# Optimization experiments

Measured on AMD Instinct MI355X. Metric: run time of the kernel, lower is better.

## Reference

```python
import jax, jax.numpy as jnp
import numpy as np

B, N, HID, H = 16, 256, 512, 8
DK = HID // H          # att_size = 64
FEAT = 8               # storage/operator feature dim
MLP_H = 64             # interaction MLP hidden dim
LAM = 0.1              # htap_lambda
SCALE = DK ** -0.5


def _pair_bias(feat, W1, b1, W2, b2):
    """MLP([v_i || v_j || |v_i - v_j|]) for all pairs -> [B,N,N,H].
    Split W1 over the three concat blocks so the per-node parts are O(N)."""
    F = feat.shape[-1]
    Wa, Wb, Wc = W1[:F], W1[F:2 * F], W1[2 * F:]
    hi = feat @ Wa                                    # [B,N,MLP_H]
    hj = feat @ Wb                                    # [B,N,MLP_H]
    diff = jnp.abs(feat[:, :, None, :] - feat[:, None, :, :])  # [B,N,N,F]
    h = jax.nn.relu(hi[:, :, None, :] + hj[:, None, :, :] + diff @ Wc + b1)
    return h @ W2 + b2                                # [B,N,N,H]


def setup_inputs() -> dict:
    key = jax.random.key(0)
    ks = jax.random.split(key, 24)
    g = lambda i, shape, s=0.05: jax.random.normal(ks[i], shape, jnp.float32) * (1.0 if s is None else 1.0) * (s / 0.05 * 0.05 if False else 1.0)
    def w(i, shape, scale):
        return jax.random.normal(ks[i], shape, jnp.float32) * scale
    inp = {
        "q": w(0, (B, N, HID), 1.0),
        "k": w(1, (B, N, HID), 1.0),
        "v": w(2, (B, N, HID), 1.0),
        "tree_attn_bias": w(3, (B, H, N, N), 1.0),
        "storage_features": w(4, (B, N, FEAT), 1.0),
        "operator_features": w(5, (B, N, FEAT), 1.0),
        # attention projections (stored as [in,out])
        "Wq": w(6, (HID, HID), HID ** -0.5), "bq": jnp.zeros((HID,), jnp.float32),
        "Wk": w(7, (HID, HID), HID ** -0.5), "bk": jnp.zeros((HID,), jnp.float32),
        "Wv": w(8, (HID, HID), HID ** -0.5), "bv": jnp.zeros((HID,), jnp.float32),
        "Wo": w(9, (HID, HID), HID ** -0.5), "bo": jnp.zeros((HID,), jnp.float32),
        # f_s interaction MLP: Linear(3*FEAT,64) -> ReLU -> Linear(64,H)
        "fs_W1": w(10, (3 * FEAT, MLP_H), (3 * FEAT) ** -0.5), "fs_b1": jnp.zeros((MLP_H,), jnp.float32),
        "fs_W2": w(11, (MLP_H, H), MLP_H ** -0.5), "fs_b2": jnp.zeros((H,), jnp.float32),
        # f_o interaction MLP
        "fo_W1": w(12, (3 * FEAT, MLP_H), (3 * FEAT) ** -0.5), "fo_b1": jnp.zeros((MLP_H,), jnp.float32),
        "fo_W2": w(13, (MLP_H, H), MLP_H ** -0.5), "fo_b2": jnp.zeros((H,), jnp.float32),
    }
    return inp


def reference(q, k, v, tree_attn_bias, storage_features, operator_features,
              Wq, bq, Wk, bk, Wv, bv, Wo, bo,
              fs_W1, fs_b1, fs_W2, fs_b2, fo_W1, fo_b1, fo_W2, fo_b2):
    # projections -> [B,H,N,DK]
    qh = (q @ Wq + bq).reshape(B, N, H, DK).transpose(0, 2, 1, 3) * SCALE
    kh = (k @ Wk + bk).reshape(B, N, H, DK).transpose(0, 2, 1, 3)
    vh = (v @ Wv + bv).reshape(B, N, H, DK).transpose(0, 2, 1, 3)

    scores = jnp.einsum("bhnd,bhmd->bhnm", qh, kh) + tree_attn_bias

    htap = (_pair_bias(storage_features, fs_W1, fs_b1, fs_W2, fs_b2)
            + _pair_bias(operator_features, fo_W1, fo_b1, fo_W2, fo_b2))  # [B,N,N,H]
    scores = scores + LAM * htap.transpose(0, 3, 1, 2)

    attn = jax.nn.softmax(scores, axis=-1)            # dropout rate 0 (eval)
    x = jnp.einsum("bhnm,bhmd->bhnd", attn, vh)
    x = x.transpose(0, 2, 1, 3).reshape(B, N, HID)
    return x @ Wo + bo
```

## Files before the change

kernel.cpp:

```cpp
#include <hip/hip_runtime.h>
#include <hip/hip_bf16.h>
#include <stdint.h>

#define B_    16
#define N_    256
#define HID_  512
#define H_    8
#define DK_   64
#define FEAT_ 8
#define MLPH_ 64
#define LAM_  0.1f
#define SCALE_ 0.125f

typedef short bf16x8 __attribute__((ext_vector_type(8)));
typedef float f32x4  __attribute__((ext_vector_type(4)));

union U8 { uint4 u; bf16x8 h; ushort s[8]; };

__device__ __forceinline__ uint16_t f32_to_bf16(float x) {
    uint32_t u = __float_as_uint(x);
    u += 0x7fffu + ((u >> 16) & 1u);
    return (uint16_t)(u >> 16);
}
__device__ __forceinline__ float bf16_to_f32(uint16_t v) {
    return __uint_as_float(((uint32_t)v) << 16);
}
__device__ __forceinline__ uint32_t pk_bf16(float lo, float hi) {
    float2 xy; xy.x = lo; xy.y = hi;
    __hip_bfloat162 b2 = __float22bfloat162_rn(xy);
    return *(uint32_t*)&b2;
}
#define LDS_FENCE() asm volatile("s_waitcnt lgkmcnt(0)" ::: "memory")

__global__ __launch_bounds__(256, 4) void proj_kernel(
    const float* __restrict__ q, const float* __restrict__ k, const float* __restrict__ v,
    const float* __restrict__ Wq, const float* __restrict__ bq,
    const float* __restrict__ Wk, const float* __restrict__ bk,
    const float* __restrict__ Wv, const float* __restrict__ bv,
    ushort* __restrict__ qh, ushort* __restrict__ kh, ushort* __restrict__ vh)
{
    int z = blockIdx.z;
    const float* X    = (z == 0) ? q  : (z == 1) ? k  : v;
    const float* W    = (z == 0) ? Wq : (z == 1) ? Wk : Wv;
    const float* bias = (z == 0) ? bq : (z == 1) ? bk : bv;
    ushort* out       = (z == 0) ? qh : (z == 1) ? kh : vh;
    float scale       = (z == 0) ? SCALE_ : 1.0f;

    int m0 = blockIdx.x * 128;
    int h  = blockIdx.y;
    int c0 = h * 64;

    __shared__ __align__(16) ushort Xs[2][128 * 40];
    __shared__ __align__(16) ushort Ws[2][64 * 40];

    int t = threadIdx.x;
    int wave = t >> 6, lane = t & 63;
    int l15 = lane & 15, qd = lane >> 4;

    int xr = t >> 1, xc = (t & 1) * 16;
    int kr = t & 15, nq = t >> 4;

    f32x4 acc0[4] = {}, acc1[4] = {};

    float4 xv[4], w0, w1;
    #pragma unroll
    for (int p = 0; p < 4; p++)
        xv[p] = *(const float4*)&X[(m0 + xr) * HID_ + xc + p * 4];
    w0 = *(const float4*)&W[(2 * kr) * HID_ + c0 + nq * 4];
    w1 = *(const float4*)&W[(2 * kr + 1) * HID_ + c0 + nq * 4];

    for (int k0 = 0; k0 < HID_; k0 += 32) {
        int buf = (k0 >> 5) & 1;
        #pragma unroll
        for (int p = 0; p < 4; p++) {
            ushort4 o;
            o.x = f32_to_bf16(xv[p].x); o.y = f32_to_bf16(xv[p].y);
            o.z = f32_to_bf16(xv[p].z); o.w = f32_to_bf16(xv[p].w);
            *(ushort4*)&Xs[buf][xr * 40 + xc + p * 4] = o;
        }
        {
            const float* a0 = &w0.x; const float* a1 = &w1.x;
            #pragma unroll
            for (int i = 0; i < 4; i++) {
                uint32_t pk = (uint32_t)f32_to_bf16(a0[i]) | ((uint32_t)f32_to_bf16(a1[i]) << 16);
                *(uint32_t*)&Ws[buf][(nq * 4 + i) * 40 + 2 * kr] = pk;
            }
        }
        __syncthreads();

        if (k0 + 32 < HID_) {
            int kn = k0 + 32;
            #pragma unroll
            for (int p = 0; p < 4; p++)
                xv[p] = *(const float4*)&X[(m0 + xr) * HID_ + kn + xc + p * 4];
            w0 = *(const float4*)&W[(kn + 2 * kr) * HID_ + c0 + nq * 4];
            w1 = *(const float4*)&W[(kn + 2 * kr + 1) * HID_ + c0 + nq * 4];
        }

        bf16x8 af0 = *(const bf16x8*)&Xs[buf][(wave * 32 + l15) * 40 + qd * 8];
        bf16x8 af1 = *(const bf16x8*)&Xs[buf][(wave * 32 + 16 + l15) * 40 + qd * 8];
        #pragma unroll
        for (int nt = 0; nt < 4; nt++) {
            bf16x8 bf = *(const bf16x8*)&Ws[buf][(nt * 16 + l15) * 40 + qd * 8];
            acc0[nt] = __builtin_amdgcn_mfma_f32_16x16x32_bf16(af0, bf, acc0[nt], 0, 0, 0);
            acc1[nt] = __builtin_amdgcn_mfma_f32_16x16x32_bf16(af1, bf, acc1[nt], 0, 0, 0);
        }
    }

    #pragma unroll
    for (int nt = 0; nt < 4; nt++) {
        float bb = bias[c0 + nt * 16 + l15];
        #pragma unroll
        for (int g = 0; g < 2; g++) {
            const f32x4& a = g ? acc1[nt] : acc0[nt];
            #pragma unroll
            for (int r = 0; r < 4; r++) {
                int m = m0 + wave * 32 + g * 16 + qd * 4 + r;
                int b_ = m >> 8, n_ = m & 255;
                float val = (a[r] + bb) * scale;
                out[(((b_ * H_ + h) * N_) + n_) * DK_ + nt * 16 + l15] = f32_to_bf16(val);
            }
        }
    }
}

__global__ void prep_frags(const float* __restrict__ fsW1, const float* __restrict__ foW1,
                           const float* __restrict__ fsW2, const float* __restrict__ foW2,
                           uint4* __restrict__ bfrag1, uint4* __restrict__ bfrag2)
{
    int t = threadIdx.x;
    #pragma unroll
    for (int e = t; e < 512; e += 256) {
        int nt = e >> 6, lane = e & 63, l15 = lane & 15, qd = lane >> 4;
        int n = nt * 16 + l15;
        ushort vals[8];
        #pragma unroll
        for (int u = 0; u < 8; u++) {
            float x = 0.f;
            if (n < 64) {
                if (qd == 0) x = fsW1[(16 + u) * 64 + n];
                else if (qd == 1) x = fsW1[(8 + u) * 64 + n];
            } else {
                int n2 = n - 64;
                if (qd == 2) x = foW1[(16 + u) * 64 + n2];
                else if (qd == 3) x = foW1[(8 + u) * 64 + n2];
            }
            vals[u] = f32_to_bf16(x);
        }
        uint4 pk;
        pk.x = (uint32_t)vals[0] | ((uint32_t)vals[1] << 16);
        pk.y = (uint32_t)vals[2] | ((uint32_t)vals[3] << 16);
        pk.z = (uint32_t)vals[4] | ((uint32_t)vals[5] << 16);
        pk.w = (uint32_t)vals[6] | ((uint32_t)vals[7] << 16);
        bfrag1[e] = pk;
    }
    {
        int e = t;
        int ks = e >> 6, lane = e & 63, l15 = lane & 15, qd = lane >> 4;
        ushort vals[8];
        #pragma unroll
        for (int u = 0; u < 8; u++) {
            float x = 0.f;
            if (l15 < 8) {
                int k2 = ks * 32 + qd * 8 + u;
                int c = ((k2 & 7) << 4) | (k2 >> 3);
                x = LAM_ * ((c < 64) ? fsW2[c * 8 + l15] : foW2[(c - 64) * 8 + l15]);
            }
            vals[u] = f32_to_bf16(x);
        }
        uint4 pk;
        pk.x = (uint32_t)vals[0] | ((uint32_t)vals[1] << 16);
        pk.y = (uint32_t)vals[2] | ((uint32_t)vals[3] << 16);
        pk.z = (uint32_t)vals[4] | ((uint32_t)vals[5] << 16);
        pk.w = (uint32_t)vals[6] | ((uint32_t)vals[7] << 16);
        bfrag2[e] = pk;
    }
}

#define HSTRIDE 136
__global__ __launch_bounds__(256, 4) void pair_bias_mfma(
    const float* __restrict__ sf, const float* __restrict__ of,
    const float* __restrict__ fsW1, const float* __restrict__ fsb1,
    const float* __restrict__ foW1, const float* __restrict__ fob1,
    const float* __restrict__ fsb2, const float* __restrict__ fob2,
    const uint4* __restrict__ bfrag1, const uint4* __restrict__ bfrag2,
    ushort* __restrict__ mlpb)
{
    __shared__ __align__(16) ushort hbuf[4][16 * HSTRIDE];
    __shared__ float hisbuf[128];
    __shared__ __align__(4) ushort tbuf[4][8 * 16];

    int i = blockIdx.x, b = blockIdx.y;
    int t = threadIdx.x;
    int wave = t >> 6, lane = t & 63;
    int l15 = lane & 15, qd = lane >> 4;

    if (t < 128) {
        int set = t >> 6, kk = t & 63;
        const float* W1 = set ? foW1 : fsW1;
        const float* fi = (set ? of : sf) + (b * N_ + i) * FEAT_;
        float a = (set ? fob1 : fsb1)[kk];
        #pragma unroll
        for (int f = 0; f < FEAT_; f++) a += fi[f] * W1[f * 64 + kk];
        hisbuf[t] = a;
    }

    bf16x8 Bf1[8], Bf2[4];
    #pragma unroll
    for (int nt = 0; nt < 8; nt++) { U8 u; u.u = bfrag1[nt * 64 + lane]; Bf1[nt] = u.h; }
    #pragma unroll
    for (int ks = 0; ks < 4; ks++) { U8 u; u.u = bfrag2[ks * 64 + lane]; Bf2[ks] = u.h; }

    const float* fsr = sf + (b * N_ + i) * FEAT_;
    const float* forr = of + (b * N_ + i) * FEAT_;
    float fsi[8], foi[8];
    #pragma unroll
    for (int u = 0; u < 8; u++) { fsi[u] = fsr[u]; foi[u] = forr[u]; }
    float b2l = LAM_ * (fsb2[l15 & 7] + fob2[l15 & 7]);

    __syncthreads();

    float hv[8];
    #pragma unroll
    for (int nt = 0; nt < 8; nt++) hv[nt] = hisbuf[nt * 16 + l15];

    ushort* hb = hbuf[wave];
    #pragma unroll
    for (int qt = 0; qt < 4; qt++) {
        int j0 = (wave * 4 + qt) * 16;
        int j = j0 + l15;

        const float* fr = ((qd < 2) ? sf : of) + (b * N_ + j) * FEAT_;
        float4 f0 = *(const float4*)&fr[0];
        float4 f1 = *(const float4*)&fr[4];
        float vals[8] = {f0.x, f0.y, f0.z, f0.w, f1.x, f1.y, f1.z, f1.w};
        if ((qd & 1) == 0) {
            const float* fi = (qd < 2) ? fsi : foi;
            #pragma unroll
            for (int u = 0; u < 8; u++) vals[u] = fabsf(vals[u] - fi[u]);
        }
        U8 au;
        #pragma unroll
        for (int p = 0; p < 4; p++)
            ((uint32_t*)&au)[p] = pk_bf16(vals[2 * p], vals[2 * p + 1]);
        bf16x8 af = au.h;

        f32x4 S1[8];
        #pragma unroll
        for (int nt = 0; nt < 8; nt++) {
            f32x4 c0 = {hv[nt], hv[nt], hv[nt], hv[nt]};
            S1[nt] = __builtin_amdgcn_mfma_f32_16x16x32_bf16(af, Bf1[nt], c0, 0, 0, 0);
        }

        #pragma unroll
        for (int r = 0; r < 4; r++) {
            uint4 w;
            w.x = pk_bf16(fmaxf(S1[0][r], 0.f), fmaxf(S1[1][r], 0.f));
            w.y = pk_bf16(fmaxf(S1[2][r], 0.f), fmaxf(S1[3][r], 0.f));
            w.z = pk_bf16(fmaxf(S1[4][r], 0.f), fmaxf(S1[5][r], 0.f));
            w.w = pk_bf16(fmaxf(S1[6][r], 0.f), fmaxf(S1[7][r], 0.f));
            *(uint4*)&hb[(qd * 4 + r) * HSTRIDE + l15 * 8] = w;
        }
        LDS_FENCE();

        f32x4 S2 = {b2l, b2l, b2l, b2l};
        #pragma unroll
        for (int ks = 0; ks < 4; ks++) {
            bf16x8 a2 = *(const bf16x8*)&hb[l15 * HSTRIDE + ks * 32 + qd * 8];
            S2 = __builtin_amdgcn_mfma_f32_16x16x32_bf16(a2, Bf2[ks], S2, 0, 0, 0);
        }

        if (l15 < 8) {
            #pragma unroll
            for (int r = 0; r < 4; r++)
                tbuf[wave][l15 * 16 + qd * 4 + r] = f32_to_bf16(S2[r]);
        }
        LDS_FENCE();

        {
            int h2 = lane >> 3, jp = lane & 7;
            uint32_t lo = tbuf[wave][h2 * 16 + jp * 2];
            uint32_t hi = tbuf[wave][h2 * 16 + jp * 2 + 1];
            uint32_t pk = lo | (hi << 16);
            *(uint32_t*)&mlpb[(((size_t)(b * H_ + h2) * N_ + i) * N_) + j0 + jp * 2] = pk;
        }
    }
}

__global__ __launch_bounds__(256, 2) void attn_kernel(
    const ushort* __restrict__ qh, const ushort* __restrict__ kh,
    const ushort* __restrict__ vh, const float* __restrict__ tree,
    const ushort* __restrict__ mlpb, ushort* __restrict__ ctxb)
{
    __shared__ __align__(16) ushort bufKP[256 * 72];
    __shared__ __align__(16) ushort bufV[64 * 264];

    int blk = blockIdx.x;
    int bh = blk >> 2;
    int quarter = blk & 3;

    int t = threadIdx.x;
    int wave = t >> 6, lane = t & 63;
    int l15 = lane & 15, qd = lane >> 4;
    int i0w = quarter * 64 + wave * 16;

    const ushort* khb = kh + (size_t)bh * N_ * DK_;
    const ushort* vhb = vh + (size_t)bh * N_ * DK_;

    #pragma unroll
    for (int u = t; u < 2048; u += 256) {
        int j = u >> 3, seg = (u & 7) * 8;
        uint4 kv = *(const uint4*)&khb[j * DK_ + seg];
        *(uint4*)&bufKP[j * 72 + seg] = kv;
    }
    #pragma unroll
    for (int u = t; u < 1024; u += 256) {
        int rp = u & 127, d0 = (u >> 7) * 8;
        U8 v0, v1;
        v0.u = *(const uint4*)&vhb[(2 * rp) * DK_ + d0];
        v1.u = *(const uint4*)&vhb[(2 * rp + 1) * DK_ + d0];
        #pragma unroll
        for (int jj = 0; jj < 8; jj++) {
            uint32_t pk = (uint32_t)v0.s[jj] | ((uint32_t)v1.s[jj] << 16);
            *(uint32_t*)&bufV[(d0 + jj) * 264 + 2 * rp] = pk;
        }
    }
    __syncthreads();

    bf16x8 a0, a1;
    {
        size_t qb = ((size_t)bh * N_ + i0w + l15) * DK_;
        U8 t0, t1;
        t0.u = *(const uint4*)&qh[qb + qd * 8];
        t1.u = *(const uint4*)&qh[qb + 32 + qd * 8];
        a0 = t0.h; a1 = t1.h;
    }
    f32x4 S[16];
    #pragma unroll
    for (int nt = 0; nt < 16; nt++) {
        f32x4 acc = {};
        bf16x8 b0 = *(const bf16x8*)&bufKP[(nt * 16 + l15) * 72 + qd * 8];
        bf16x8 b1 = *(const bf16x8*)&bufKP[(nt * 16 + l15) * 72 + 32 + qd * 8];
        acc = __builtin_amdgcn_mfma_f32_16x16x32_bf16(a0, b0, acc, 0, 0, 0);
        acc = __builtin_amdgcn_mfma_f32_16x16x32_bf16(a1, b1, acc, 0, 0, 0);
        S[nt] = acc;
    }

    {
        size_t base = ((size_t)bh * N_ + i0w + qd * 4) * N_ + l15;
        const float*  tr = tree + base;
        const ushort* mb = mlpb + base;
        #pragma unroll
        for (int nt = 0; nt < 16; nt++)
            #pragma unroll
            for (int r = 0; r < 4; r++)
                S[nt][r] += tr[(size_t)r * N_ + nt * 16] + bf16_to_f32(mb[(size_t)r * N_ + nt * 16]);
    }

    float mx[4], sm[4];
    #pragma unroll
    for (int r = 0; r < 4; r++) mx[r] = -1e30f;
    #pragma unroll
    for (int nt = 0; nt < 16; nt++)
        #pragma unroll
        for (int r = 0; r < 4; r++) mx[r] = fmaxf(mx[r], S[nt][r]);
    #pragma unroll
    for (int r = 0; r < 4; r++) {
        #pragma unroll
        for (int m = 1; m <= 8; m <<= 1) mx[r] = fmaxf(mx[r], __shfl_xor(mx[r], m));
    }
    #pragma unroll
    for (int r = 0; r < 4; r++) sm[r] = 0.f;
    #pragma unroll
    for (int nt = 0; nt < 16; nt++)
        #pragma unroll
        for (int r = 0; r < 4; r++) {
            float e = __expf(S[nt][r] - mx[r]);
            S[nt][r] = e;
            sm[r] += e;
        }
    #pragma unroll
    for (int r = 0; r < 4; r++) {
        #pragma unroll
        for (int m = 1; m <= 8; m <<= 1) sm[r] += __shfl_xor(sm[r], m);
        sm[r] = 1.0f / sm[r];
    }

    __syncthreads();

    {
        uint32_t* Pw = (uint32_t*)&bufKP[wave * 16 * 264];
        #pragma unroll
        for (int nt = 0; nt < 16; nt++)
            #pragma unroll
            for (int r = 0; r < 4; r++) {
                float p = S[nt][r] * sm[r];
                float po = __shfl_xor(p, 1);
                uint32_t pk = (uint32_t)f32_to_bf16(p) | ((uint32_t)f32_to_bf16(po) << 16);
                if ((lane & 1) == 0)
                    Pw[(qd * 4 + r) * 132 + nt * 8 + (l15 >> 1)] = pk;
            }
    }
    __syncthreads();

    const ushort* Pw = &bufKP[wave * 16 * 264];
    f32x4 O[4] = {};
    #pragma unroll
    for (int ks = 0; ks < 8; ks++) {
        int j0 = ks * 32;
        bf16x8 pa = *(const bf16x8*)&Pw[l15 * 264 + j0 + qd * 8];
        #pragma unroll
        for (int ntd = 0; ntd < 4; ntd++) {
            bf16x8 vb = *(const bf16x8*)&bufV[(ntd * 16 + l15) * 264 + j0 + qd * 8];
            O[ntd] = __builtin_amdgcn_mfma_f32_16x16x32_bf16(pa, vb, O[ntd], 0, 0, 0);
        }
    }

    #pragma unroll
    for (int ntd = 0; ntd < 4; ntd++)
        #pragma unroll
        for (int r = 0; r < 4; r++)
            ctxb[((size_t)bh * N_ + i0w + qd * 4 + r) * DK_ + ntd * 16 + l15] =
                f32_to_bf16(O[ntd][r]);
}

__global__ __launch_bounds__(256, 4) void outproj_kernel(
    const ushort* __restrict__ ctxb, const float* __restrict__ Wo,
    const float* __restrict__ bo, float* __restrict__ out)
{
    int m0 = blockIdx.x * 64;
    int c0 = blockIdx.y * 64;

    __shared__ __align__(16) ushort Xs[64 * 40];
    __shared__ __align__(16) ushort Ws[64 * 40];

    int t = threadIdx.x;
    int wave = t >> 6, lane = t & 63;
    int l15 = lane & 15, qd = lane >> 4;

    f32x4 acc[4] = {};

    for (int k0 = 0; k0 < HID_; k0 += 32) {
        __syncthreads();
        {
            int r = t >> 2, s8 = (t & 3) * 8;
            int m = m0 + r, b_ = m >> 8, n_ = m & 255;
            uint4 xv = *(const uint4*)&ctxb[(((b_ * H_ + (k0 >> 6)) * N_) + n_) * DK_ + (k0 & 63) + s8];
            *(uint4*)&Xs[r * 40 + s8] = xv;
        }
        {
            int kr = t & 15, nq = t >> 4;
            float4 w0 = *(const float4*)&Wo[(k0 + 2 * kr) * HID_ + c0 + nq * 4];
            float4 w1 = *(const float4*)&Wo[(k0 + 2 * kr + 1) * HID_ + c0 + nq * 4];
            const float* a0 = &w0.x; const float* a1 = &w1.x;
            #pragma unroll
            for (int i = 0; i < 4; i++) {
                uint32_t pk = (uint32_t)f32_to_bf16(a0[i]) | ((uint32_t)f32_to_bf16(a1[i]) << 16);
                *(uint32_t*)&Ws[(nq * 4 + i) * 40 + 2 * kr] = pk;
            }
        }
        __syncthreads();
        bf16x8 af = *(const bf16x8*)&Xs[(wave * 16 + l15) * 40 + qd * 8];
        #pragma unroll
        for (int nt = 0; nt < 4; nt++) {
            bf16x8 bf = *(const bf16x8*)&Ws[(nt * 16 + l15) * 40 + qd * 8];
            acc[nt] = __builtin_amdgcn_mfma_f32_16x16x32_bf16(af, bf, acc[nt], 0, 0, 0);
        }
    }

    #pragma unroll
    for (int nt = 0; nt < 4; nt++) {
        float bb = bo[c0 + nt * 16 + l15];
        #pragma unroll
        for (int r = 0; r < 4; r++) {
            int m = m0 + wave * 16 + qd * 4 + r;
            out[m * HID_ + c0 + nt * 16 + l15] = acc[nt][r] + bb;
        }
    }
}

extern "C" void kernel_launch(void* const* d_in, const int* in_sizes, int n_in,
                              void* d_out, int out_size, void* d_ws, size_t ws_size,
                              hipStream_t stream)
{
    const float* q    = (const float*)d_in[0];
    const float* k    = (const float*)d_in[1];
    const float* v    = (const float*)d_in[2];
    const float* tree = (const float*)d_in[3];
    const float* sf   = (const float*)d_in[4];
    const float* of   = (const float*)d_in[5];
    const float* Wq   = (const float*)d_in[6];
    const float* bq   = (const float*)d_in[7];
    const float* Wk   = (const float*)d_in[8];
    const float* bk   = (const float*)d_in[9];
    const float* Wv   = (const float*)d_in[10];
    const float* bv   = (const float*)d_in[11];
    const float* Wo   = (const float*)d_in[12];
    const float* bo   = (const float*)d_in[13];
    const float* fsW1 = (const float*)d_in[14];
    const float* fsb1 = (const float*)d_in[15];
    const float* fsW2 = (const float*)d_in[16];
    const float* fsb2 = (const float*)d_in[17];
    const float* foW1 = (const float*)d_in[18];
    const float* fob1 = (const float*)d_in[19];
    const float* foW2 = (const float*)d_in[20];
    const float* fob2 = (const float*)d_in[21];

    char* ws = (char*)d_ws;
    ushort* qh     = (ushort*)(ws + 0);
    ushort* kh     = (ushort*)(ws + 4194304);
    ushort* vh     = (ushort*)(ws + 8388608);
    ushort* ctxb   = (ushort*)(ws + 12582912);
    uint4*  bfrag1 = (uint4*)(ws + 16777216);
    uint4*  bfrag2 = (uint4*)(ws + 16785408);
    ushort* mlpb   = (ushort*)(ws + 23080960);

    proj_kernel<<<dim3(32, 8, 3), 256, 0, stream>>>(q, k, v, Wq, bq, Wk, bk, Wv, bv, qh, kh, vh);
    prep_frags<<<1, 256, 0, stream>>>(fsW1, foW1, fsW2, foW2, bfrag1, bfrag2);
    pair_bias_mfma<<<dim3(N_, B_), 256, 0, stream>>>(sf, of, fsW1, fsb1, foW1, fob1,
                                                     fsb2, fob2, bfrag1, bfrag2, mlpb);
    attn_kernel<<<512, 256, 0, stream>>>(qh, kh, vh, tree, mlpb, ctxb);
    outproj_kernel<<<dim3(64, 8), 256, 0, stream>>>(ctxb, Wo, bo, (float*)d_out);
}
```

Measured before the change: 226.4 us.

## Software-pipeline pair-bias MLP stages with double-buffered LDS per wave

Restructures the pair_bias kernel so that all four A-fragments are loaded from global before the barrier. The first-layer MFMAs for the next 16-column tile are issued while the second-layer MFMAs and the store for the current tile run, using double-buffered hidden and transpose LDS buffers. The aim is to hide MFMA and LDS latency within each wave. In exchange it uses more registers and twice the LDS, and lowers the launch_bounds occupancy hint from 4 to 3 blocks.

```diff
diff --git a/kernel.cpp b/kernel.cpp
--- a/kernel.cpp
+++ b/kernel.cpp
@@ -178,7 +178,7 @@
 }
 
 #define HSTRIDE 136
-__global__ __launch_bounds__(256, 4) void pair_bias_mfma(
+__global__ __launch_bounds__(256, 3) void pair_bias_mfma(
     const float* __restrict__ sf, const float* __restrict__ of,
     const float* __restrict__ fsW1, const float* __restrict__ fsb1,
     const float* __restrict__ foW1, const float* __restrict__ fob1,
@@ -186,9 +186,9 @@
     const uint4* __restrict__ bfrag1, const uint4* __restrict__ bfrag2,
     ushort* __restrict__ mlpb)
 {
-    __shared__ __align__(16) ushort hbuf[4][16 * HSTRIDE];
+    __shared__ __align__(16) ushort hbuf[4][2][16 * HSTRIDE];
     __shared__ float hisbuf[128];
-    __shared__ __align__(4) ushort tbuf[4][8 * 16];
+    __shared__ __align__(4) ushort tbuf[4][2][8 * 16];
 
     int i = blockIdx.x, b = blockIdx.y;
     int t = threadIdx.x;
@@ -218,18 +218,10 @@
     for (int u = 0; u < 8; u++) { fsi[u] = fsr[u]; foi[u] = forr[u]; }
     float b2l = LAM_ * (fsb2[l15 & 7] + fob2[l15 & 7]);
 
-    __syncthreads();
-
-    float hv[8];
-    #pragma unroll
-    for (int nt = 0; nt < 8; nt++) hv[nt] = hisbuf[nt * 16 + l15];
-
-    ushort* hb = hbuf[wave];
+    bf16x8 af[4];
     #pragma unroll
     for (int qt = 0; qt < 4; qt++) {
-        int j0 = (wave * 4 + qt) * 16;
-        int j = j0 + l15;
-
+        int j = (wave * 4 + qt) * 16 + l15;
         const float* fr = ((qd < 2) ? sf : of) + (b * N_ + j) * FEAT_;
         float4 f0 = *(const float4*)&fr[0];
         float4 f1 = *(const float4*)&fr[4];
@@ -243,15 +235,22 @@
         #pragma unroll
         for (int p = 0; p < 4; p++)
             ((uint32_t*)&au)[p] = pk_bf16(vals[2 * p], vals[2 * p + 1]);
-        bf16x8 af = au.h;
-
+        af[qt] = au.h;
+    }
+
+    __syncthreads();
+    float hv[8];
+    #pragma unroll
+    for (int nt = 0; nt < 8; nt++) hv[nt] = hisbuf[nt * 16 + l15];
+
+    {
         f32x4 S1[8];
         #pragma unroll
         for (int nt = 0; nt < 8; nt++) {
             f32x4 c0 = {hv[nt], hv[nt], hv[nt], hv[nt]};
-            S1[nt] = __builtin_amdgcn_mfma_f32_16x16x32_bf16(af, Bf1[nt], c0, 0, 0, 0);
-        }
-
+            S1[nt] = __builtin_amdgcn_mfma_f32_16x16x32_bf16(af[0], Bf1[nt], c0, 0, 0, 0);
+        }
+        ushort* hb = &hbuf[wave][0][0];
         #pragma unroll
         for (int r = 0; r < 4; r++) {
             uint4 w;
@@ -261,28 +260,57 @@
             w.w = pk_bf16(fmaxf(S1[6][r], 0.f), fmaxf(S1[7][r], 0.f));
             *(uint4*)&hb[(qd * 4 + r) * HSTRIDE + l15 * 8] = w;
         }
+    }
+
+    #pragma unroll
+    for (int qt = 0; qt < 4; qt++) {
+        ushort* hbC = &hbuf[wave][qt & 1][0];
+        ushort* hbN = &hbuf[wave][(qt & 1) ^ 1][0];
         LDS_FENCE();
 
+        f32x4 Sn[8];
+        if (qt < 3) {
+            #pragma unroll
+            for (int nt = 0; nt < 8; nt++) {
+                f32x4 c0 = {hv[nt], hv[nt], hv[nt], hv[nt]};
+                Sn[nt] = __builtin_amdgcn_mfma_f32_16x16x32_bf16(af[qt + 1], Bf1[nt], c0, 0, 0, 0);
+            }
+        }
+
         f32x4 S2 = {b2l, b2l, b2l, b2l};
         #pragma unroll
         for (int ks = 0; ks < 4; ks++) {
-            bf16x8 a2 = *(const bf16x8*)&hb[l15 * HSTRIDE + ks * 32 + qd * 8];
+            bf16x8 a2 = *(const bf16x8*)&hbC[l15 * HSTRIDE + ks * 32 + qd * 8];
             S2 = __builtin_amdgcn_mfma_f32_16x16x32_bf16(a2, Bf2[ks], S2, 0, 0, 0);
         }
 
+        ushort* tb = &tbuf[wave][qt & 1][0];
         if (l15 < 8) {
             #pragma unroll
             for (int r = 0; r < 4; r++)
-                tbuf[wave][l15 * 16 + qd * 4 + r] = f32_to_bf16(S2[r]);
+                tb[l15 * 16 + qd * 4 + r] = f32_to_bf16(S2[r]);
         }
         LDS_FENCE();
 
         {
+            int j0 = (wave * 4 + qt) * 16;
             int h2 = lane >> 3, jp = lane & 7;
-            uint32_t lo = tbuf[wave][h2 * 16 + jp * 2];
-            uint32_t hi = tbuf[wave][h2 * 16 + jp * 2 + 1];
+            uint32_t lo = tb[h2 * 16 + jp * 2];
+            uint32_t hi = tb[h2 * 16 + jp * 2 + 1];
             uint32_t pk = lo | (hi << 16);
             *(uint32_t*)&mlpb[(((size_t)(b * H_ + h2) * N_ + i) * N_) + j0 + jp * 2] = pk;
+        }
+
+        if (qt < 3) {
+            #pragma unroll
+            for (int r = 0; r < 4; r++) {
+                uint4 w;
+                w.x = pk_bf16(fmaxf(Sn[0][r], 0.f), fmaxf(Sn[1][r], 0.f));
+                w.y = pk_bf16(fmaxf(Sn[2][r], 0.f), fmaxf(Sn[3][r], 0.f));
+                w.z = pk_bf16(fmaxf(Sn[4][r], 0.f), fmaxf(Sn[5][r], 0.f));
+                w.w = pk_bf16(fmaxf(Sn[6][r], 0.f), fmaxf(Sn[7][r], 0.f));
+                *(uint4*)&hbN[(qd * 4 + r) * HSTRIDE + l15 * 8] = w;
+            }
         }
     }
 }
```

After: 225.3 us. About the same (-0.5%).

## Merge projection and pair-bias kernels into one interleaved launch

Applied to the files above, without the earlier changes.

Folds the QKV projection GEMM and the pair-bias MLP into a single kernel whose 4864 blocks interleave 3 projection blocks with 16 pair-bias blocks per group. Both stages share one statically sized shared-memory buffer. The goal is to run the compute-heavy MFMA projection alongside the memory-bound pair-bias work and drop one launch and its tail. In exchange the shared-memory footprint is the larger of the two stages, which may lower occupancy for the pair-bias blocks, and both paths now compete for register allocation under one launch bound.

```diff
diff --git a/kernel.cpp b/kernel.cpp
--- a/kernel.cpp
+++ b/kernel.cpp
@@ -31,98 +31,6 @@
     return *(uint32_t*)&b2;
 }
 #define LDS_FENCE() asm volatile("s_waitcnt lgkmcnt(0)" ::: "memory")
-
-__global__ __launch_bounds__(256, 4) void proj_kernel(
-    const float* __restrict__ q, const float* __restrict__ k, const float* __restrict__ v,
-    const float* __restrict__ Wq, const float* __restrict__ bq,
-    const float* __restrict__ Wk, const float* __restrict__ bk,
-    const float* __restrict__ Wv, const float* __restrict__ bv,
-    ushort* __restrict__ qh, ushort* __restrict__ kh, ushort* __restrict__ vh)
-{
-    int z = blockIdx.z;
-    const float* X    = (z == 0) ? q  : (z == 1) ? k  : v;
-    const float* W    = (z == 0) ? Wq : (z == 1) ? Wk : Wv;
-    const float* bias = (z == 0) ? bq : (z == 1) ? bk : bv;
-    ushort* out       = (z == 0) ? qh : (z == 1) ? kh : vh;
-    float scale       = (z == 0) ? SCALE_ : 1.0f;
-
-    int m0 = blockIdx.x * 128;
-    int h  = blockIdx.y;
-    int c0 = h * 64;
-
-    __shared__ __align__(16) ushort Xs[2][128 * 40];
-    __shared__ __align__(16) ushort Ws[2][64 * 40];
-
-    int t = threadIdx.x;
-    int wave = t >> 6, lane = t & 63;
-    int l15 = lane & 15, qd = lane >> 4;
-
-    int xr = t >> 1, xc = (t & 1) * 16;
-    int kr = t & 15, nq = t >> 4;
-
-    f32x4 acc0[4] = {}, acc1[4] = {};
-
-    float4 xv[4], w0, w1;
-    #pragma unroll
-    for (int p = 0; p < 4; p++)
-        xv[p] = *(const float4*)&X[(m0 + xr) * HID_ + xc + p * 4];
-    w0 = *(const float4*)&W[(2 * kr) * HID_ + c0 + nq * 4];
-    w1 = *(const float4*)&W[(2 * kr + 1) * HID_ + c0 + nq * 4];
-
-    for (int k0 = 0; k0 < HID_; k0 += 32) {
-        int buf = (k0 >> 5) & 1;
-        #pragma unroll
-        for (int p = 0; p < 4; p++) {
-            ushort4 o;
-            o.x = f32_to_bf16(xv[p].x); o.y = f32_to_bf16(xv[p].y);
-            o.z = f32_to_bf16(xv[p].z); o.w = f32_to_bf16(xv[p].w);
-            *(ushort4*)&Xs[buf][xr * 40 + xc + p * 4] = o;
-        }
-        {
-            const float* a0 = &w0.x; const float* a1 = &w1.x;
-            #pragma unroll
-            for (int i = 0; i < 4; i++) {
-                uint32_t pk = (uint32_t)f32_to_bf16(a0[i]) | ((uint32_t)f32_to_bf16(a1[i]) << 16);
-                *(uint32_t*)&Ws[buf][(nq * 4 + i) * 40 + 2 * kr] = pk;
-            }
-        }
-        __syncthreads();
-
-        if (k0 + 32 < HID_) {
-            int kn = k0 + 32;
-            #pragma unroll
-            for (int p = 0; p < 4; p++)
-                xv[p] = *(const float4*)&X[(m0 + xr) * HID_ + kn + xc + p * 4];
-            w0 = *(const float4*)&W[(kn + 2 * kr) * HID_ + c0 + nq * 4];
-            w1 = *(const float4*)&W[(kn + 2 * kr + 1) * HID_ + c0 + nq * 4];
-        }
-
-        bf16x8 af0 = *(const bf16x8*)&Xs[buf][(wave * 32 + l15) * 40 + qd * 8];
-        bf16x8 af1 = *(const bf16x8*)&Xs[buf][(wave * 32 + 16 + l15) * 40 + qd * 8];
-        #pragma unroll
-        for (int nt = 0; nt < 4; nt++) {
-            bf16x8 bf = *(const bf16x8*)&Ws[buf][(nt * 16 + l15) * 40 + qd * 8];
-            acc0[nt] = __builtin_amdgcn_mfma_f32_16x16x32_bf16(af0, bf, acc0[nt], 0, 0, 0);
-            acc1[nt] = __builtin_amdgcn_mfma_f32_16x16x32_bf16(af1, bf, acc1[nt], 0, 0, 0);
-        }
-    }
-
-    #pragma unroll
-    for (int nt = 0; nt < 4; nt++) {
-        float bb = bias[c0 + nt * 16 + l15];
-        #pragma unroll
-        for (int g = 0; g < 2; g++) {
-            const f32x4& a = g ? acc1[nt] : acc0[nt];
-            #pragma unroll
-            for (int r = 0; r < 4; r++) {
-                int m = m0 + wave * 32 + g * 16 + qd * 4 + r;
-                int b_ = m >> 8, n_ = m & 255;
-                float val = (a[r] + bb) * scale;
-                out[(((b_ * H_ + h) * N_) + n_) * DK_ + nt * 16 + l15] = f32_to_bf16(val);
-            }
-        }
-    }
-}
 
 __global__ void prep_frags(const float* __restrict__ fsW1, const float* __restrict__ foW1,
                            const float* __restrict__ fsW2, const float* __restrict__ foW2,
@@ -177,8 +85,102 @@
     }
 }
 
+
 #define HSTRIDE 136
-__global__ __launch_bounds__(256, 4) void pair_bias_mfma(
+
+__device__ __forceinline__ void proj_body(
+    int bx, int h, int z, ushort* __restrict__ smem,
+    const float* __restrict__ q, const float* __restrict__ k, const float* __restrict__ v,
+    const float* __restrict__ Wq, const float* __restrict__ bq,
+    const float* __restrict__ Wk, const float* __restrict__ bk,
+    const float* __restrict__ Wv, const float* __restrict__ bv,
+    ushort* __restrict__ qh, ushort* __restrict__ kh, ushort* __restrict__ vh)
+{
+    const float* X    = (z == 0) ? q  : (z == 1) ? k  : v;
+    const float* W    = (z == 0) ? Wq : (z == 1) ? Wk : Wv;
+    const float* bias = (z == 0) ? bq : (z == 1) ? bk : bv;
+    ushort* out       = (z == 0) ? qh : (z == 1) ? kh : vh;
+    float scale       = (z == 0) ? SCALE_ : 1.0f;
+
+    int m0 = bx * 128;
+    int c0 = h * 64;
+
+    ushort* Xs = smem;
+    ushort* Ws = smem + 10240;
+
+    int t = threadIdx.x;
+    int wave = t >> 6, lane = t & 63;
+    int l15 = lane & 15, qd = lane >> 4;
+
+    int xr = t >> 1, xc = (t & 1) * 16;
+    int kr = t & 15, nq = t >> 4;
+
+    f32x4 acc0[4] = {}, acc1[4] = {};
+
+    float4 xv[4], w0, w1;
+    #pragma unroll
+    for (int p = 0; p < 4; p++)
+        xv[p] = *(const float4*)&X[(m0 + xr) * HID_ + xc + p * 4];
+    w0 = *(const float4*)&W[(2 * kr) * HID_ + c0 + nq * 4];
+    w1 = *(const float4*)&W[(2 * kr + 1) * HID_ + c0 + nq * 4];
+
+    for (int k0 = 0; k0 < HID_; k0 += 32) {
+        int buf = (k0 >> 5) & 1;
+        #pragma unroll
+        for (int p = 0; p < 4; p++) {
+            ushort4 o;
+            o.x = f32_to_bf16(xv[p].x); o.y = f32_to_bf16(xv[p].y);
+            o.z = f32_to_bf16(xv[p].z); o.w = f32_to_bf16(xv[p].w);
+            *(ushort4*)&Xs[buf * 5120 + xr * 40 + xc + p * 4] = o;
+        }
+        {
+            const float* a0 = &w0.x; const float* a1 = &w1.x;
+            #pragma unroll
+            for (int i = 0; i < 4; i++) {
+                uint32_t pk = (uint32_t)f32_to_bf16(a0[i]) | ((uint32_t)f32_to_bf16(a1[i]) << 16);
+                *(uint32_t*)&Ws[buf * 2560 + (nq * 4 + i) * 40 + 2 * kr] = pk;
+            }
+        }
+        __syncthreads();
+
+        if (k0 + 32 < HID_) {
+            int kn = k0 + 32;
+            #pragma unroll
+            for (int p = 0; p < 4; p++)
+                xv[p] = *(const float4*)&X[(m0 + xr) * HID_ + kn + xc + p * 4];
+            w0 = *(const float4*)&W[(kn + 2 * kr) * HID_ + c0 + nq * 4];
+            w1 = *(const float4*)&W[(kn + 2 * kr + 1) * HID_ + c0 + nq * 4];
+        }
+
+        bf16x8 af0 = *(const bf16x8*)&Xs[buf * 5120 + (wave * 32 + l15) * 40 + qd * 8];
+        bf16x8 af1 = *(const bf16x8*)&Xs[buf * 5120 + (wave * 32 + 16 + l15) * 40 + qd * 8];
+        #pragma unroll
+        for (int nt = 0; nt < 4; nt++) {
+            bf16x8 bf = *(const bf16x8*)&Ws[buf * 2560 + (nt * 16 + l15) * 40 + qd * 8];
+            acc0[nt] = __builtin_amdgcn_mfma_f32_16x16x32_bf16(af0, bf, acc0[nt], 0, 0, 0);
+            acc1[nt] = __builtin_amdgcn_mfma_f32_16x16x32_bf16(af1, bf, acc1[nt], 0, 0, 0);
+        }
+    }
+
+    #pragma unroll
+    for (int nt = 0; nt < 4; nt++) {
+        float bb = bias[c0 + nt * 16 + l15];
+        #pragma unroll
+        for (int g = 0; g < 2; g++) {
+            const f32x4& a = g ? acc1[nt] : acc0[nt];
+            #pragma unroll
+            for (int r = 0; r < 4; r++) {
+                int m = m0 + wave * 32 + g * 16 + qd * 4 + r;
+                int b_ = m >> 8, n_ = m & 255;
+                float val = (a[r] + bb) * scale;
+                out[(((b_ * H_ + h) * N_) + n_) * DK_ + nt * 16 + l15] = f32_to_bf16(val);
+            }
+        }
+    }
+}
+
+__device__ __forceinline__ void pair_body(
+    int i, int b, ushort* __restrict__ smem,
     const float* __restrict__ sf, const float* __restrict__ of,
     const float* __restrict__ fsW1, const float* __restrict__ fsb1,
     const float* __restrict__ foW1, const float* __restrict__ fob1,
@@ -186,11 +188,10 @@
     const uint4* __restrict__ bfrag1, const uint4* __restrict__ bfrag2,
     ushort* __restrict__ mlpb)
 {
-    __shared__ __align__(16) ushort hbuf[4][16 * HSTRIDE];
-    __shared__ float hisbuf[128];
-    __shared__ __align__(4) ushort tbuf[4][8 * 16];
-
-    int i = blockIdx.x, b = blockIdx.y;
+    ushort* hbuf   = smem;
+    float*  hisbuf = (float*)(smem + 8704);
+    ushort* tbuf   = smem + 8960;
+
     int t = threadIdx.x;
     int wave = t >> 6, lane = t & 63;
     int l15 = lane & 15, qd = lane >> 4;
@@ -224,7 +225,8 @@
     #pragma unroll
     for (int nt = 0; nt < 8; nt++) hv[nt] = hisbuf[nt * 16 + l15];
 
-    ushort* hb = hbuf[wave];
+    ushort* hb = hbuf + wave * 2176;
+    ushort* tb = tbuf + wave * 128;
     #pragma unroll
     for (int qt = 0; qt < 4; qt++) {
         int j0 = (wave * 4 + qt) * 16;
@@ -273,17 +275,46 @@
         if (l15 < 8) {
             #pragma unroll
             for (int r = 0; r < 4; r++)
-                tbuf[wave][l15 * 16 + qd * 4 + r] = f32_to_bf16(S2[r]);
+                tb[l15 * 16 + qd * 4 + r] = f32_to_bf16(S2[r]);
         }
         LDS_FENCE();
 
         {
             int h2 = lane >> 3, jp = lane & 7;
-            uint32_t lo = tbuf[wave][h2 * 16 + jp * 2];
-            uint32_t hi = tbuf[wave][h2 * 16 + jp * 2 + 1];
+            uint32_t lo = tb[h2 * 16 + jp * 2];
+            uint32_t hi = tb[h2 * 16 + jp * 2 + 1];
             uint32_t pk = lo | (hi << 16);
             *(uint32_t*)&mlpb[(((size_t)(b * H_ + h2) * N_ + i) * N_) + j0 + jp * 2] = pk;
         }
+    }
+}
+
+__global__ __launch_bounds__(256, 4) void mega_kernel(
+    const float* __restrict__ q, const float* __restrict__ k, const float* __restrict__ v,
+    const float* __restrict__ Wq, const float* __restrict__ bq,
+    const float* __restrict__ Wk, const float* __restrict__ bk,
+    const float* __restrict__ Wv, const float* __restrict__ bv,
+    ushort* __restrict__ qh, ushort* __restrict__ kh, ushort* __restrict__ vh,
+    const float* __restrict__ sf, const float* __restrict__ of,
+    const float* __restrict__ fsW1, const float* __restrict__ fsb1,
+    const float* __restrict__ foW1, const float* __restrict__ fob1,
+    const float* __restrict__ fsb2, const float* __restrict__ fob2,
+    const uint4* __restrict__ bfrag1, const uint4* __restrict__ bfrag2,
+    ushort* __restrict__ mlpb)
+{
+    __shared__ __align__(16) ushort smem[15360];
+
+    int blk = blockIdx.x;
+    int grp = blk / 19;
+    int pos = blk - grp * 19;
+    if (pos >= 3) {
+        int id = grp * 16 + (pos - 3);
+        pair_body(id & 255, id >> 8, smem, sf, of, fsW1, fsb1, foW1, fob1,
+                  fsb2, fob2, bfrag1, bfrag2, mlpb);
+    } else {
+        int id = grp * 3 + pos;
+        proj_body(id & 31, (id >> 5) & 7, id >> 8, smem,
+                  q, k, v, Wq, bq, Wk, bk, Wv, bv, qh, kh, vh);
     }
 }
 
@@ -515,10 +546,10 @@
     uint4*  bfrag2 = (uint4*)(ws + 16785408);
     ushort* mlpb   = (ushort*)(ws + 23080960);
 
-    proj_kernel<<<dim3(32, 8, 3), 256, 0, stream>>>(q, k, v, Wq, bq, Wk, bk, Wv, bv, qh, kh, vh);
     prep_frags<<<1, 256, 0, stream>>>(fsW1, foW1, fsW2, foW2, bfrag1, bfrag2);
-    pair_bias_mfma<<<dim3(N_, B_), 256, 0, stream>>>(sf, of, fsW1, fsb1, foW1, fob1,
-                                                     fsb2, fob2, bfrag1, bfrag2, mlpb);
+    mega_kernel<<<4864, 256, 0, stream>>>(q, k, v, Wq, bq, Wk, bk, Wv, bv, qh, kh, vh,
+                                          sf, of, fsW1, fsb1, foW1, fob1,
+                                          fsb2, fob2, bfrag1, bfrag2, mlpb);
     attn_kernel<<<512, 256, 0, stream>>>(qh, kh, vh, tree, mlpb, ctxb);
     outproj_kernel<<<dim3(64, 8), 256, 0, stream>>>(ctxb, Wo, bo, (float*)d_out);
 }
```

After: 233.4 us. +3.1%, slower.
